# Performance work log

Hardware: AMD Instinct MI355X
Metric: run time of the kernel (lower is better)

Reference implementation:

```python
import jax, jax.numpy as jnp
import numpy as np

E = 8       # n_experts
K = 2       # k_experts
D_IN = 1024
D_OUT = 1024
D_EXP = 2048
N = 16384   # tokens (batch*seq, forward requires 2D input)


def setup_inputs() -> dict:
    key = jax.random.key(0)
    ks = jax.random.split(key, 4)
    x = jax.random.normal(ks[0], (N, D_IN), jnp.float32)
    Wg = jax.random.normal(ks[1], (E, D_IN), jnp.float32) * 0.02      # router weight
    bg = jnp.zeros((E,), jnp.float32)                                  # router bias
    W_in = jax.random.normal(ks[2], (E, D_EXP, D_IN), jnp.float32) * 0.02
    b_in = jnp.zeros((E, D_EXP), jnp.float32)                          # w_in_bias_init=0.0
    W_out = jax.random.normal(ks[3], (E, D_OUT, D_EXP), jnp.float32) * 0.02  # bias=False
    return {"x": x, "Wg": Wg, "bg": bg, "W_in": W_in, "b_in": b_in, "W_out": W_out}


def moe_forward(x, Wg, bg, W_in, b_in, W_out):
    # Eval mode: gate jitter / solu jitter / dropouts are training-only no-ops.
    n = x.shape[0]
    # --- routing ---
    logits = x @ Wg.T + bg                                 # [N, E]
    probs = jax.nn.softmax(logits, axis=-1)
    mean_probs = probs.mean(axis=0)                        # [E]
    k_vals, k_idx = jax.lax.top_k(probs, K)                # [N, K]
    k_w = k_vals / k_vals.sum(axis=-1, keepdims=True)      # renormalized gate weights
    counts = jnp.bincount(k_idx.reshape(-1), length=E)     # [E] int
    load_balancing_loss = E * jnp.sum((counts.astype(x.dtype) / n) * mean_probs)
    # --- dispatch + expert w_in (loop over fixed small E; combine with one-hot mask) ---
    sel = jax.nn.one_hot(k_idx, E, dtype=x.dtype)          # [N, K, E]
    h = jnp.zeros((n, K, D_EXP), x.dtype)                  # preacts per (token, slot)
    for e in range(E):
        he = x @ W_in[e].T + b_in[e]                       # [N, D_EXP]
        h = h + sel[:, :, e][..., None] * he[:, None, :]
    # --- SoLU (eval): softmax(preacts) * preacts over hidden dim ---
    acts = jax.nn.softmax(h, axis=-1) * h                  # [N, K, D_EXP]
    # --- expert w_out (no bias) ---
    out = jnp.zeros((n, K, D_OUT), x.dtype)
    for e in range(E):
        oe = jnp.einsum('nkh,oh->nko', acts, W_out[e])
        out = out + sel[:, :, e][..., None] * oe
    # --- weighted combine over the K chosen experts ---
    outputs = (out * k_w[..., None]).sum(axis=1)           # [N, D_OUT]
    return outputs, load_balancing_loss


def reference(x, Wg, bg, W_in, b_in, W_out):
    return moe_forward(x, Wg, bg, W_in, b_in, W_out)
```

## Files before the change

### kernel.cpp

```cpp
#include <hip/hip_runtime.h>
#include <hip/hip_bf16.h>
#include <stdint.h>

#define E_EXP 8
#define NTOK  16384
#define DIN   1024
#define DEXP  2048
#define DOUT  1024
#define NSLOT (NTOK*2)
#define MAXT  264

typedef __attribute__((ext_vector_type(8))) short short8;
typedef __attribute__((ext_vector_type(8))) unsigned short ushort8;
typedef __attribute__((ext_vector_type(4))) float f32x4;

__device__ __forceinline__ unsigned short f2bf(float f){
  union { float f; uint32_t u; } v; v.f = f;
  uint32_t r = (v.u + 0x7FFFu + ((v.u >> 16) & 1u)) >> 16;
  return (unsigned short)r;
}
__device__ __forceinline__ float bf2f(unsigned short u){
  union { uint32_t u; float f; } v; v.u = ((uint32_t)u) << 16;
  return v.f;
}

__device__ __forceinline__ void async16(const void* g, void* l){
  __builtin_amdgcn_global_load_lds(
      (const __attribute__((address_space(1))) void*)g,
      (__attribute__((address_space(3))) void*)l, 16, 0, 0);
}

#define VMCNT8() asm volatile("s_waitcnt vmcnt(8)" ::: "memory")
#define VMCNT0() asm volatile("s_waitcnt vmcnt(0)" ::: "memory")
#define BARRIER() do { asm volatile("" ::: "memory"); __builtin_amdgcn_s_barrier(); asm volatile("" ::: "memory"); } while(0)

__global__ __launch_bounds__(256) void cast_bf16(const float* __restrict__ s,
                                                 unsigned short* __restrict__ d, int n){
  int i = (blockIdx.x*256 + threadIdx.x)*8;
  if (i >= n) return;
  float4 a = *(const float4*)(s+i);
  float4 b = *(const float4*)(s+i+4);
  ushort8 o;
  o[0]=f2bf(a.x); o[1]=f2bf(a.y); o[2]=f2bf(a.z); o[3]=f2bf(a.w);
  o[4]=f2bf(b.x); o[5]=f2bf(b.y); o[6]=f2bf(b.z); o[7]=f2bf(b.w);
  *(ushort8*)(d+i) = o;
}

__global__ __launch_bounds__(256) void router(
    const float* __restrict__ x, const float* __restrict__ Wg, const float* __restrict__ bg,
    int* __restrict__ eidx, float* __restrict__ gw,
    int* __restrict__ counts, float* __restrict__ probsum)
{
  __shared__ float sWg[E_EXP*DIN];
  __shared__ float sps[E_EXP];
  __shared__ int   scnt[E_EXP];
  const int tid = threadIdx.x;
  for (int i = tid; i < E_EXP*DIN; i += 256) sWg[i] = Wg[i];
  if (tid < E_EXP){ sps[tid]=0.f; scnt[tid]=0; }
  __syncthreads();
  const int lane = tid & 63;
  const int wv   = tid >> 6;
  for (int it = 0; it < 16; ++it){
    const int token = blockIdx.x*64 + wv*16 + it;
    float4 xv[4];
#pragma unroll
    for (int j=0;j<4;++j) xv[j] = *(const float4*)&x[(size_t)token*DIN + j*256 + lane*4];
    float p[E_EXP];
#pragma unroll
    for (int e2=0;e2<E_EXP;++e2){
      float s = 0.f;
#pragma unroll
      for (int j=0;j<4;++j){
        const float4 w4 = *(const float4*)&sWg[e2*DIN + j*256 + lane*4];
        s += xv[j].x*w4.x + xv[j].y*w4.y + xv[j].z*w4.z + xv[j].w*w4.w;
      }
      p[e2] = s;
    }
#pragma unroll
    for (int d=1; d<64; d<<=1){
#pragma unroll
      for (int e2=0;e2<E_EXP;++e2) p[e2] += __shfl_xor(p[e2], d);
    }
    if (lane == 0){
      float mx = -1e30f;
#pragma unroll
      for (int e2=0;e2<E_EXP;++e2){ p[e2] += bg[e2]; mx = fmaxf(mx, p[e2]); }
      float se = 0.f;
#pragma unroll
      for (int e2=0;e2<E_EXP;++e2){ p[e2] = __expf(p[e2]-mx); se += p[e2]; }
      const float inv = 1.f/se;
#pragma unroll
      for (int e2=0;e2<E_EXP;++e2){ p[e2] *= inv; atomicAdd(&sps[e2], p[e2]); }
      int i1 = 0;
#pragma unroll
      for (int e2=1;e2<E_EXP;++e2) if (p[e2] > p[i1]) i1 = e2;
      int i2 = (i1==0) ? 1 : 0;
#pragma unroll
      for (int e2=0;e2<E_EXP;++e2) if (e2 != i1 && p[e2] > p[i2]) i2 = e2;
      const float v1 = p[i1], v2 = p[i2], s12 = v1 + v2;
      eidx[2*token]   = i1; eidx[2*token+1] = i2;
      gw[2*token]     = v1/s12; gw[2*token+1] = v2/s12;
      atomicAdd(&scnt[i1], 1); atomicAdd(&scnt[i2], 1);
    }
  }
  __syncthreads();
  if (tid < E_EXP){ atomicAdd(&counts[tid], scnt[tid]); atomicAdd(&probsum[tid], sps[tid]); }
}

__global__ void finalize(const int* __restrict__ counts, const float* __restrict__ probsum,
                         float* __restrict__ loss_out, int* __restrict__ offs,
                         int* __restrict__ cursor, int* __restrict__ tile_e,
                         int* __restrict__ tile_row, int* __restrict__ ntiles)
{
  if (threadIdx.x != 0 || blockIdx.x != 0) return;
  int off = 0, nt = 0;
  float loss = 0.f;
  offs[0] = 0;
  for (int e2=0;e2<E_EXP;++e2){
    const int c = counts[e2];
    loss += (float)c * probsum[e2];
    cursor[e2] = 0;
    const int t = (c + 127) >> 7;
    for (int i=0;i<t;++i){ tile_e[nt] = e2; tile_row[nt] = off + i*128; ++nt; }
    off += c;
    offs[e2+1] = off;
  }
  *ntiles = nt;
  *loss_out = loss * (8.f/((float)NTOK*(float)NTOK));
}

__global__ __launch_bounds__(256) void scatter(const int* __restrict__ eidx, const float* __restrict__ gw,
    const int* __restrict__ offs, int* __restrict__ cursor,
    int* __restrict__ ptok, float* __restrict__ pw)
{
  const int t = blockIdx.x*256 + threadIdx.x;
  if (t >= NTOK) return;
#pragma unroll
  for (int s=0;s<2;++s){
    const int e2  = eidx[2*t+s];
    const int pos = offs[e2] + atomicAdd(&cursor[e2], 1);
    ptok[pos] = t;
    pw[pos]   = gw[2*t+s];
  }
}

__global__ __launch_bounds__(256) void gemm1(
    const unsigned short* __restrict__ xb,
    const unsigned short* __restrict__ wib,
    const float* __restrict__ b_in,
    unsigned short* __restrict__ H,
    const int* __restrict__ ptok,
    const int* __restrict__ offs,
    const int* __restrict__ tile_e,
    const int* __restrict__ tile_row,
    const int* __restrict__ ntiles)
{
  if ((int)blockIdx.x >= *ntiles) return;
  const int e    = tile_e[blockIdx.x];
  const int row0 = tile_row[blockIdx.x];
  const int seg_end = offs[e+1];
  const int col0 = blockIdx.y * 128;

  __shared__ unsigned short As[2][128*64];
  __shared__ unsigned short Bs[2][128*64];

  const int tid  = threadIdx.x;
  const int lane = tid & 63;
  const int wv   = tid >> 6;
  const int wm   = wv >> 1, wn = wv & 1;
  const int crow = lane >> 3;
  const int cks  = ((lane & 7) ^ crow) * 8;

  const unsigned short* ag[4];
  const unsigned short* bg4[4];
  unsigned int alo[4], blo[4];
#pragma unroll
  for (int i = 0; i < 4; ++i){
    const int chunk = wv*4 + i;
    const int row = chunk*8 + crow;
    int g = row0 + row; if (g > NSLOT-1) g = NSLOT-1;
    const int tok = ptok[g];
    ag[i]  = xb + (size_t)tok*DIN + cks;
    bg4[i] = wib + ((size_t)e*DEXP + col0 + row)*DIN + cks;
    alo[i] = chunk*512;
    blo[i] = chunk*512;
  }

  f32x4 acc[4][4] = {};
  const int NK = DIN/64;
  int cur = 0;

#pragma unroll
  for (int i = 0; i < 4; ++i){
    async16(ag[i],  &As[0][alo[i]]);
    async16(bg4[i], &Bs[0][blo[i]]);
  }

#pragma unroll 2
  for (int kt = 0; kt < NK; ++kt){
    BARRIER();
    if (kt + 1 < NK){
      const int ko = (kt+1)*64;
#pragma unroll
      for (int i = 0; i < 4; ++i){
        async16(ag[i]  + ko, &As[cur^1][alo[i]]);
        async16(bg4[i] + ko, &Bs[cur^1][blo[i]]);
      }
      VMCNT8();
    } else {
      VMCNT0();
    }
    BARRIER();

    __builtin_amdgcn_s_setprio(1);
#pragma unroll
    for (int kk = 0; kk < 2; ++kk){
      const int ksl = ((kk*4 + (lane>>4)) ^ (lane & 7)) * 8;
      short8 a[4], b[4];
#pragma unroll
      for (int m = 0; m < 4; ++m)
        a[m] = *(const short8*)&As[cur][(wm*64 + m*16 + (lane&15))*64 + ksl];
#pragma unroll
      for (int n = 0; n < 4; ++n)
        b[n] = *(const short8*)&Bs[cur][(wn*64 + n*16 + (lane&15))*64 + ksl];
#pragma unroll
      for (int m = 0; m < 4; ++m)
#pragma unroll
        for (int n = 0; n < 4; ++n)
          acc[m][n] = __builtin_amdgcn_mfma_f32_16x16x32_bf16(a[m], b[n], acc[m][n], 0, 0, 0);
    }
    __builtin_amdgcn_s_setprio(0);
    cur ^= 1;
  }

  float bias[4];
#pragma unroll
  for (int n = 0; n < 4; ++n)
    bias[n] = b_in[e*DEXP + col0 + wn*64 + n*16 + (lane&15)];

#pragma unroll
  for (int m = 0; m < 4; ++m){
#pragma unroll
    for (int j = 0; j < 4; ++j){
      const int r = wm*64 + m*16 + (lane>>4)*4 + j;
      const int g = row0 + r;
      if (g < seg_end){
#pragma unroll
        for (int n = 0; n < 4; ++n){
          const int c = col0 + wn*64 + n*16 + (lane&15);
          H[(size_t)g*DEXP + c] = f2bf(acc[m][n][j] + bias[n]);
        }
      }
    }
  }
}

__global__ __launch_bounds__(256) void solu(unsigned short* __restrict__ H){
  const size_t row = blockIdx.x;
  unsigned short* hp = H + row*DEXP;
  const int tid  = threadIdx.x;
  const int lane = tid & 63;
  const int wv   = tid >> 6;
  const short8 hv = *(const short8*)&hp[tid*8];
  float f[8];
#pragma unroll
  for (int j=0;j<8;++j) f[j] = bf2f((unsigned short)hv[j]);
  float mx = f[0];
#pragma unroll
  for (int j=1;j<8;++j) mx = fmaxf(mx, f[j]);
  for (int d=1; d<64; d<<=1) mx = fmaxf(mx, __shfl_xor(mx, d));
  __shared__ float redm[4];
  __shared__ float reds[4];
  if (lane==0) redm[wv] = mx;
  __syncthreads();
  mx = fmaxf(fmaxf(redm[0],redm[1]), fmaxf(redm[2],redm[3]));
  float se = 0.f; float ex[8];
#pragma unroll
  for (int j=0;j<8;++j){ ex[j] = __expf(f[j]-mx); se += ex[j]; }
  for (int d=1; d<64; d<<=1) se += __shfl_xor(se, d);
  if (lane==0) reds[wv] = se;
  __syncthreads();
  se = reds[0]+reds[1]+reds[2]+reds[3];
  const float inv = 1.0f/se;
  ushort8 o;
#pragma unroll
  for (int j=0;j<8;++j) o[j] = f2bf(f[j]*ex[j]*inv);
  *(ushort8*)&hp[tid*8] = o;
}

__global__ __launch_bounds__(256) void gemm2(
    const unsigned short* __restrict__ ACT,
    const unsigned short* __restrict__ wob,
    float* __restrict__ out,
    const int* __restrict__ ptok,
    const float* __restrict__ pw,
    const int* __restrict__ offs,
    const int* __restrict__ tile_e,
    const int* __restrict__ tile_row,
    const int* __restrict__ ntiles)
{
  if ((int)blockIdx.x >= *ntiles) return;
  const int e    = tile_e[blockIdx.x];
  const int row0 = tile_row[blockIdx.x];
  const int seg_end = offs[e+1];
  const int col0 = blockIdx.y * 128;

  __shared__ unsigned short As[2][128*64];
  __shared__ unsigned short Bs[2][128*64];

  const int tid  = threadIdx.x;
  const int lane = tid & 63;
  const int wv   = tid >> 6;
  const int wm   = wv >> 1, wn = wv & 1;
  const int crow = lane >> 3;
  const int cks  = ((lane & 7) ^ crow) * 8;

  const unsigned short* ag[4];
  const unsigned short* bg4[4];
  unsigned int alo[4], blo[4];
#pragma unroll
  for (int i = 0; i < 4; ++i){
    const int chunk = wv*4 + i;
    const int row = chunk*8 + crow;
    int g = row0 + row; if (g > NSLOT-1) g = NSLOT-1;
    ag[i]  = ACT + (size_t)g*DEXP + cks;
    bg4[i] = wob + ((size_t)e*DOUT + col0 + row)*DEXP + cks;
    alo[i] = chunk*512;
    blo[i] = chunk*512;
  }

  f32x4 acc[4][4] = {};
  const int NK = DEXP/64;
  int cur = 0;

#pragma unroll
  for (int i = 0; i < 4; ++i){
    async16(ag[i],  &As[0][alo[i]]);
    async16(bg4[i], &Bs[0][blo[i]]);
  }

#pragma unroll 2
  for (int kt = 0; kt < NK; ++kt){
    BARRIER();
    if (kt + 1 < NK){
      const int ko = (kt+1)*64;
#pragma unroll
      for (int i = 0; i < 4; ++i){
        async16(ag[i]  + ko, &As[cur^1][alo[i]]);
        async16(bg4[i] + ko, &Bs[cur^1][blo[i]]);
      }
      VMCNT8();
    } else {
      VMCNT0();
    }
    BARRIER();

    __builtin_amdgcn_s_setprio(1);
#pragma unroll
    for (int kk = 0; kk < 2; ++kk){
      const int ksl = ((kk*4 + (lane>>4)) ^ (lane & 7)) * 8;
      short8 a[4], b[4];
#pragma unroll
      for (int m = 0; m < 4; ++m)
        a[m] = *(const short8*)&As[cur][(wm*64 + m*16 + (lane&15))*64 + ksl];
#pragma unroll
      for (int n = 0; n < 4; ++n)
        b[n] = *(const short8*)&Bs[cur][(wn*64 + n*16 + (lane&15))*64 + ksl];
#pragma unroll
      for (int m = 0; m < 4; ++m)
#pragma unroll
        for (int n = 0; n < 4; ++n)
          acc[m][n] = __builtin_amdgcn_mfma_f32_16x16x32_bf16(a[m], b[n], acc[m][n], 0, 0, 0);
    }
    __builtin_amdgcn_s_setprio(0);
    cur ^= 1;
  }

#pragma unroll
  for (int m = 0; m < 4; ++m){
#pragma unroll
    for (int j = 0; j < 4; ++j){
      const int r = wm*64 + m*16 + (lane>>4)*4 + j;
      const int g = row0 + r;
      if (g < seg_end){
        const int tok   = ptok[g];
        const float wgt = pw[g];
        float* op = out + (size_t)tok*DOUT;
#pragma unroll
        for (int n = 0; n < 4; ++n){
          const int c = col0 + wn*64 + n*16 + (lane&15);
          unsafeAtomicAdd(op + c, wgt * acc[m][n][j]);
        }
      }
    }
  }
}

extern "C" void kernel_launch(void* const* d_in, const int* in_sizes, int n_in,
                              void* d_out, int out_size, void* d_ws, size_t ws_size,
                              hipStream_t stream)
{
  const float* x     = (const float*)d_in[0];
  const float* Wg    = (const float*)d_in[1];
  const float* bgp   = (const float*)d_in[2];
  const float* W_in  = (const float*)d_in[3];
  const float* b_in  = (const float*)d_in[4];
  const float* W_out = (const float*)d_in[5];
  float* out = (float*)d_out;

  char* base = (char*)d_ws;
  size_t o = 0;
  unsigned short* xb  = (unsigned short*)(base + o); o += (size_t)NTOK*DIN*2;
  unsigned short* wib = (unsigned short*)(base + o); o += (size_t)E_EXP*DEXP*DIN*2;
  unsigned short* wob = (unsigned short*)(base + o); o += (size_t)E_EXP*DOUT*DEXP*2;
  unsigned short* H   = (unsigned short*)(base + o); o += (size_t)NSLOT*DEXP*2;
  int*   eidx    = (int*)(base + o);   o += (size_t)NSLOT*4;
  float* gw      = (float*)(base + o); o += (size_t)NSLOT*4;
  int*   ptok    = (int*)(base + o);   o += (size_t)NSLOT*4;
  float* pw      = (float*)(base + o); o += (size_t)NSLOT*4;
  int*   counts  = (int*)(base + o);   o += 32;
  float* probsum = (float*)(base + o); o += 32;
  int*   cursor  = (int*)(base + o);   o += 32;
  int*   offs    = (int*)(base + o);   o += 64;
  int*   tile_e  = (int*)(base + o);   o += (size_t)MAXT*4;
  int*   tile_row= (int*)(base + o);   o += (size_t)MAXT*4;
  int*   ntiles  = (int*)(base + o);   o += 64;

  hipMemsetAsync(d_out, 0, (size_t)(NTOK*(size_t)DOUT + 1)*4, stream);
  hipMemsetAsync(counts, 0, 96, stream);

  cast_bf16<<<dim3(8192), 256, 0, stream>>>(x,     xb,  NTOK*DIN);
  cast_bf16<<<dim3(8192), 256, 0, stream>>>(W_in,  wib, E_EXP*DEXP*DIN);
  cast_bf16<<<dim3(8192), 256, 0, stream>>>(W_out, wob, E_EXP*DOUT*DEXP);

  router<<<dim3(256), 256, 0, stream>>>(x, Wg, bgp, eidx, gw, counts, probsum);
  finalize<<<dim3(1), 64, 0, stream>>>(counts, probsum, out + (size_t)NTOK*DOUT,
                                       offs, cursor, tile_e, tile_row, ntiles);
  scatter<<<dim3(64), 256, 0, stream>>>(eidx, gw, offs, cursor, ptok, pw);

  gemm1<<<dim3(MAXT, DEXP/128), 256, 0, stream>>>(xb, wib, b_in, H, ptok, offs,
                                                  tile_e, tile_row, ntiles);
  solu<<<dim3(NSLOT), 256, 0, stream>>>(H);
  gemm2<<<dim3(MAXT, DOUT/128), 256, 0, stream>>>(H, wob, out, ptok, pw, offs,
                                                  tile_e, tile_row, ntiles);
}
```

Before: 871.3 us.

## Widen GEMM tiles, fuse x cast into router, replace atomics with combine kernel

```diff
diff --git a/kernel.cpp b/kernel.cpp
--- a/kernel.cpp
+++ b/kernel.cpp
@@ -12,6 +12,7 @@
 
 typedef __attribute__((ext_vector_type(8))) short short8;
 typedef __attribute__((ext_vector_type(8))) unsigned short ushort8;
+typedef __attribute__((ext_vector_type(4))) unsigned short ushort4v;
 typedef __attribute__((ext_vector_type(4))) float f32x4;
 
 __device__ __forceinline__ unsigned short f2bf(float f){
@@ -30,7 +31,7 @@
       (__attribute__((address_space(3))) void*)l, 16, 0, 0);
 }
 
-#define VMCNT8() asm volatile("s_waitcnt vmcnt(8)" ::: "memory")
+#define VMCNT6() asm volatile("s_waitcnt vmcnt(6)" ::: "memory")
 #define VMCNT0() asm volatile("s_waitcnt vmcnt(0)" ::: "memory")
 #define BARRIER() do { asm volatile("" ::: "memory"); __builtin_amdgcn_s_barrier(); asm volatile("" ::: "memory"); } while(0)
 
@@ -48,6 +49,7 @@
 
 __global__ __launch_bounds__(256) void router(
     const float* __restrict__ x, const float* __restrict__ Wg, const float* __restrict__ bg,
+    unsigned short* __restrict__ xb,
     int* __restrict__ eidx, float* __restrict__ gw,
     int* __restrict__ counts, float* __restrict__ probsum)
 {
@@ -65,6 +67,12 @@
     float4 xv[4];
 #pragma unroll
     for (int j=0;j<4;++j) xv[j] = *(const float4*)&x[(size_t)token*DIN + j*256 + lane*4];
+#pragma unroll
+    for (int j=0;j<4;++j){
+      ushort4v o;
+      o[0]=f2bf(xv[j].x); o[1]=f2bf(xv[j].y); o[2]=f2bf(xv[j].z); o[3]=f2bf(xv[j].w);
+      *(ushort4v*)&xb[(size_t)token*DIN + j*256 + lane*4] = o;
+    }
     float p[E_EXP];
 #pragma unroll
     for (int e2=0;e2<E_EXP;++e2){
@@ -129,9 +137,9 @@
   *loss_out = loss * (8.f/((float)NTOK*(float)NTOK));
 }
 
-__global__ __launch_bounds__(256) void scatter(const int* __restrict__ eidx, const float* __restrict__ gw,
+__global__ __launch_bounds__(256) void scatter(const int* __restrict__ eidx,
     const int* __restrict__ offs, int* __restrict__ cursor,
-    int* __restrict__ ptok, float* __restrict__ pw)
+    int* __restrict__ ptok, int* __restrict__ inv)
 {
   const int t = blockIdx.x*256 + threadIdx.x;
   if (t >= NTOK) return;
@@ -140,11 +148,11 @@
     const int e2  = eidx[2*t+s];
     const int pos = offs[e2] + atomicAdd(&cursor[e2], 1);
     ptok[pos] = t;
-    pw[pos]   = gw[2*t+s];
-  }
-}
-
-__global__ __launch_bounds__(256) void gemm1(
+    inv[2*t+s] = pos;
+  }
+}
+
+__global__ __launch_bounds__(512, 2) void gemm1(
     const unsigned short* __restrict__ xb,
     const unsigned short* __restrict__ wib,
     const float* __restrict__ b_in,
@@ -155,46 +163,47 @@
     const int* __restrict__ tile_row,
     const int* __restrict__ ntiles)
 {
-  if ((int)blockIdx.x >= *ntiles) return;
-  const int e    = tile_e[blockIdx.x];
-  const int row0 = tile_row[blockIdx.x];
+  if ((int)blockIdx.y >= *ntiles) return;
+  const int e    = tile_e[blockIdx.y];
+  const int row0 = tile_row[blockIdx.y];
   const int seg_end = offs[e+1];
-  const int col0 = blockIdx.y * 128;
+  const int col0 = blockIdx.x * 256;
 
   __shared__ unsigned short As[2][128*64];
-  __shared__ unsigned short Bs[2][128*64];
+  __shared__ unsigned short Bs[2][256*64];
 
   const int tid  = threadIdx.x;
   const int lane = tid & 63;
   const int wv   = tid >> 6;
-  const int wm   = wv >> 1, wn = wv & 1;
-  const int crow = lane >> 3;
-  const int cks  = ((lane & 7) ^ crow) * 8;
-
-  const unsigned short* ag[4];
+  const int wm   = wv >> 2;
+  const int wn   = wv & 3;
+  const int srow = tid >> 3;
+  const int scol = ((tid & 7) ^ (srow & 7)) * 8;
+
+  const unsigned short* ag[2];
+#pragma unroll
+  for (int i = 0; i < 2; ++i){
+    int g = row0 + i*64 + srow; if (g > NSLOT-1) g = NSLOT-1;
+    const int tok = ptok[g];
+    ag[i] = xb + (size_t)tok*DIN + scol;
+  }
   const unsigned short* bg4[4];
-  unsigned int alo[4], blo[4];
-#pragma unroll
-  for (int i = 0; i < 4; ++i){
-    const int chunk = wv*4 + i;
-    const int row = chunk*8 + crow;
-    int g = row0 + row; if (g > NSLOT-1) g = NSLOT-1;
-    const int tok = ptok[g];
-    ag[i]  = xb + (size_t)tok*DIN + cks;
-    bg4[i] = wib + ((size_t)e*DEXP + col0 + row)*DIN + cks;
-    alo[i] = chunk*512;
-    blo[i] = chunk*512;
-  }
+#pragma unroll
+  for (int i = 0; i < 4; ++i)
+    bg4[i] = wib + ((size_t)e*DEXP + col0 + i*64 + srow)*DIN + scol;
+  float bias[4];
+#pragma unroll
+  for (int n = 0; n < 4; ++n)
+    bias[n] = b_in[e*DEXP + col0 + wn*64 + n*16 + (lane&15)];
 
   f32x4 acc[4][4] = {};
   const int NK = DIN/64;
   int cur = 0;
 
 #pragma unroll
-  for (int i = 0; i < 4; ++i){
-    async16(ag[i],  &As[0][alo[i]]);
-    async16(bg4[i], &Bs[0][blo[i]]);
-  }
+  for (int i = 0; i < 2; ++i) async16(ag[i],  &As[0][(i*64 + wv*8)*64]);
+#pragma unroll
+  for (int i = 0; i < 4; ++i) async16(bg4[i], &Bs[0][(i*64 + wv*8)*64]);
 
 #pragma unroll 2
   for (int kt = 0; kt < NK; ++kt){
@@ -202,11 +211,10 @@
     if (kt + 1 < NK){
       const int ko = (kt+1)*64;
 #pragma unroll
-      for (int i = 0; i < 4; ++i){
-        async16(ag[i]  + ko, &As[cur^1][alo[i]]);
-        async16(bg4[i] + ko, &Bs[cur^1][blo[i]]);
-      }
-      VMCNT8();
+      for (int i = 0; i < 2; ++i) async16(ag[i]  + ko, &As[cur^1][(i*64 + wv*8)*64]);
+#pragma unroll
+      for (int i = 0; i < 4; ++i) async16(bg4[i] + ko, &Bs[cur^1][(i*64 + wv*8)*64]);
+      VMCNT6();
     } else {
       VMCNT0();
     }
@@ -232,11 +240,6 @@
     __builtin_amdgcn_s_setprio(0);
     cur ^= 1;
   }
-
-  float bias[4];
-#pragma unroll
-  for (int n = 0; n < 4; ++n)
-    bias[n] = b_in[e*DEXP + col0 + wn*64 + n*16 + (lane&15)];
 
 #pragma unroll
   for (int m = 0; m < 4; ++m){
@@ -288,56 +291,51 @@
   *(ushort8*)&hp[tid*8] = o;
 }
 
-__global__ __launch_bounds__(256) void gemm2(
+__global__ __launch_bounds__(512, 2) void gemm2(
     const unsigned short* __restrict__ ACT,
     const unsigned short* __restrict__ wob,
-    float* __restrict__ out,
-    const int* __restrict__ ptok,
-    const float* __restrict__ pw,
+    unsigned short* __restrict__ Oslot,
     const int* __restrict__ offs,
     const int* __restrict__ tile_e,
     const int* __restrict__ tile_row,
     const int* __restrict__ ntiles)
 {
-  if ((int)blockIdx.x >= *ntiles) return;
-  const int e    = tile_e[blockIdx.x];
-  const int row0 = tile_row[blockIdx.x];
+  if ((int)blockIdx.y >= *ntiles) return;
+  const int e    = tile_e[blockIdx.y];
+  const int row0 = tile_row[blockIdx.y];
   const int seg_end = offs[e+1];
-  const int col0 = blockIdx.y * 128;
+  const int col0 = blockIdx.x * 256;
 
   __shared__ unsigned short As[2][128*64];
-  __shared__ unsigned short Bs[2][128*64];
+  __shared__ unsigned short Bs[2][256*64];
 
   const int tid  = threadIdx.x;
   const int lane = tid & 63;
   const int wv   = tid >> 6;
-  const int wm   = wv >> 1, wn = wv & 1;
-  const int crow = lane >> 3;
-  const int cks  = ((lane & 7) ^ crow) * 8;
-
-  const unsigned short* ag[4];
+  const int wm   = wv >> 2;
+  const int wn   = wv & 3;
+  const int srow = tid >> 3;
+  const int scol = ((tid & 7) ^ (srow & 7)) * 8;
+
+  const unsigned short* ag[2];
+#pragma unroll
+  for (int i = 0; i < 2; ++i){
+    int g = row0 + i*64 + srow; if (g > NSLOT-1) g = NSLOT-1;
+    ag[i] = ACT + (size_t)g*DEXP + scol;
+  }
   const unsigned short* bg4[4];
-  unsigned int alo[4], blo[4];
-#pragma unroll
-  for (int i = 0; i < 4; ++i){
-    const int chunk = wv*4 + i;
-    const int row = chunk*8 + crow;
-    int g = row0 + row; if (g > NSLOT-1) g = NSLOT-1;
-    ag[i]  = ACT + (size_t)g*DEXP + cks;
-    bg4[i] = wob + ((size_t)e*DOUT + col0 + row)*DEXP + cks;
-    alo[i] = chunk*512;
-    blo[i] = chunk*512;
-  }
+#pragma unroll
+  for (int i = 0; i < 4; ++i)
+    bg4[i] = wob + ((size_t)e*DOUT + col0 + i*64 + srow)*DEXP + scol;
 
   f32x4 acc[4][4] = {};
   const int NK = DEXP/64;
   int cur = 0;
 
 #pragma unroll
-  for (int i = 0; i < 4; ++i){
-    async16(ag[i],  &As[0][alo[i]]);
-    async16(bg4[i], &Bs[0][blo[i]]);
-  }
+  for (int i = 0; i < 2; ++i) async16(ag[i],  &As[0][(i*64 + wv*8)*64]);
+#pragma unroll
+  for (int i = 0; i < 4; ++i) async16(bg4[i], &Bs[0][(i*64 + wv*8)*64]);
 
 #pragma unroll 2
   for (int kt = 0; kt < NK; ++kt){
@@ -345,11 +343,10 @@
     if (kt + 1 < NK){
       const int ko = (kt+1)*64;
 #pragma unroll
-      for (int i = 0; i < 4; ++i){
-        async16(ag[i]  + ko, &As[cur^1][alo[i]]);
-        async16(bg4[i] + ko, &Bs[cur^1][blo[i]]);
-      }
-      VMCNT8();
+      for (int i = 0; i < 2; ++i) async16(ag[i]  + ko, &As[cur^1][(i*64 + wv*8)*64]);
+#pragma unroll
+      for (int i = 0; i < 4; ++i) async16(bg4[i] + ko, &Bs[cur^1][(i*64 + wv*8)*64]);
+      VMCNT6();
     } else {
       VMCNT0();
     }
@@ -383,15 +380,42 @@
       const int r = wm*64 + m*16 + (lane>>4)*4 + j;
       const int g = row0 + r;
       if (g < seg_end){
-        const int tok   = ptok[g];
-        const float wgt = pw[g];
-        float* op = out + (size_t)tok*DOUT;
 #pragma unroll
         for (int n = 0; n < 4; ++n){
           const int c = col0 + wn*64 + n*16 + (lane&15);
-          unsafeAtomicAdd(op + c, wgt * acc[m][n][j]);
+          Oslot[(size_t)g*DOUT + c] = f2bf(acc[m][n][j]);
         }
       }
+    }
+  }
+}
+
+__global__ __launch_bounds__(256) void combine(const unsigned short* __restrict__ Oslot,
+    const int* __restrict__ inv, const float* __restrict__ gw, float* __restrict__ out)
+{
+  const int t    = blockIdx.x*4 + (threadIdx.x >> 6);
+  const int lane = threadIdx.x & 63;
+  const int p0 = inv[2*t], p1 = inv[2*t+1];
+  const float w0 = gw[2*t], w1 = gw[2*t+1];
+  const unsigned short* r0 = Oslot + (size_t)p0*DOUT + lane*16;
+  const unsigned short* r1 = Oslot + (size_t)p1*DOUT + lane*16;
+  ushort8 a0 = *(const ushort8*)r0;
+  ushort8 a1 = *(const ushort8*)(r0 + 8);
+  ushort8 b0 = *(const ushort8*)r1;
+  ushort8 b1 = *(const ushort8*)(r1 + 8);
+  float* op = out + (size_t)t*DOUT + lane*16;
+  float4 o;
+#pragma unroll
+  for (int q = 0; q < 2; ++q){
+    const ushort8 ua = q ? a1 : a0;
+    const ushort8 ub = q ? b1 : b0;
+#pragma unroll
+    for (int h = 0; h < 2; ++h){
+      o.x = w0*bf2f(ua[h*4+0]) + w1*bf2f(ub[h*4+0]);
+      o.y = w0*bf2f(ua[h*4+1]) + w1*bf2f(ub[h*4+1]);
+      o.z = w0*bf2f(ua[h*4+2]) + w1*bf2f(ub[h*4+2]);
+      o.w = w0*bf2f(ua[h*4+3]) + w1*bf2f(ub[h*4+3]);
+      *(float4*)(op + q*8 + h*4) = o;
     }
   }
 }
@@ -414,10 +438,11 @@
   unsigned short* wib = (unsigned short*)(base + o); o += (size_t)E_EXP*DEXP*DIN*2;
   unsigned short* wob = (unsigned short*)(base + o); o += (size_t)E_EXP*DOUT*DEXP*2;
   unsigned short* H   = (unsigned short*)(base + o); o += (size_t)NSLOT*DEXP*2;
+  unsigned short* Oslot = (unsigned short*)d_ws;
   int*   eidx    = (int*)(base + o);   o += (size_t)NSLOT*4;
   float* gw      = (float*)(base + o); o += (size_t)NSLOT*4;
   int*   ptok    = (int*)(base + o);   o += (size_t)NSLOT*4;
-  float* pw      = (float*)(base + o); o += (size_t)NSLOT*4;
+  int*   inv     = (int*)(base + o);   o += (size_t)NSLOT*4;
   int*   counts  = (int*)(base + o);   o += 32;
   float* probsum = (float*)(base + o); o += 32;
   int*   cursor  = (int*)(base + o);   o += 32;
@@ -426,21 +451,20 @@
   int*   tile_row= (int*)(base + o);   o += (size_t)MAXT*4;
   int*   ntiles  = (int*)(base + o);   o += 64;
 
-  hipMemsetAsync(d_out, 0, (size_t)(NTOK*(size_t)DOUT + 1)*4, stream);
   hipMemsetAsync(counts, 0, 96, stream);
 
-  cast_bf16<<<dim3(8192), 256, 0, stream>>>(x,     xb,  NTOK*DIN);
   cast_bf16<<<dim3(8192), 256, 0, stream>>>(W_in,  wib, E_EXP*DEXP*DIN);
   cast_bf16<<<dim3(8192), 256, 0, stream>>>(W_out, wob, E_EXP*DOUT*DEXP);
 
-  router<<<dim3(256), 256, 0, stream>>>(x, Wg, bgp, eidx, gw, counts, probsum);
+  router<<<dim3(256), 256, 0, stream>>>(x, Wg, bgp, xb, eidx, gw, counts, probsum);
   finalize<<<dim3(1), 64, 0, stream>>>(counts, probsum, out + (size_t)NTOK*DOUT,
                                        offs, cursor, tile_e, tile_row, ntiles);
-  scatter<<<dim3(64), 256, 0, stream>>>(eidx, gw, offs, cursor, ptok, pw);
-
-  gemm1<<<dim3(MAXT, DEXP/128), 256, 0, stream>>>(xb, wib, b_in, H, ptok, offs,
+  scatter<<<dim3(64), 256, 0, stream>>>(eidx, offs, cursor, ptok, inv);
+
+  gemm1<<<dim3(DEXP/256, MAXT), 512, 0, stream>>>(xb, wib, b_in, H, ptok, offs,
                                                   tile_e, tile_row, ntiles);
   solu<<<dim3(NSLOT), 256, 0, stream>>>(H);
-  gemm2<<<dim3(MAXT, DOUT/128), 256, 0, stream>>>(H, wob, out, ptok, pw, offs,
+  gemm2<<<dim3(DOUT/256, MAXT), 512, 0, stream>>>(H, wob, Oslot, offs,
                                                   tile_e, tile_row, ntiles);
-}
+  combine<<<dim3(NTOK/4), 256, 0, stream>>>(Oslot, inv, gw, out);
+}
```

New measurement: 792.7 us. -9.0%, faster.
